# Performance work log

Measured on AMD Instinct MI355X. Metric: run time of the kernel, lower is better.

## Reference

```python
import jax, jax.numpy as jnp
import numpy as np

WIDTH, HEIGHT = 256, 256
FOV = 1.0471975511965976  # 60 deg horizontal fov, radians
Z_NEAR, Z_FAR = 2.0, 6.0
NUM_SAMPLES = 64
HIDDEN = 64


def get_cam_ray_dirs(width, height, horizontal_fov):
    rot_y = jnp.linspace(-horizontal_fov / 2.0, horizontal_fov / 2.0, width)
    vfov = horizontal_fov * height / width
    rot_x = jnp.linspace(vfov / 2.0, -vfov / 2.0, height)
    rot_y = jnp.broadcast_to(rot_y[None, :], (height, width))
    rot_x = jnp.broadcast_to(rot_x[:, None], (height, width))
    x = -jnp.sin(rot_y) * jnp.cos(rot_x)
    y = jnp.sin(rot_x)
    z = -jnp.cos(rot_y) * jnp.cos(rot_x)
    return jnp.stack([x, y, z], axis=2)  # (H, W, 3)


def setup_inputs() -> dict:
    key = jax.random.key(0)
    k1, k2, k3, k4, k5 = jax.random.split(key, 5)
    camera_local_to_world = jax.random.normal(k1, (4, 4), dtype=jnp.float32)
    u = jax.random.uniform(k2, (HEIGHT * WIDTH, NUM_SAMPLES), dtype=jnp.float32)
    cam_ray_dirs = get_cam_ray_dirs(WIDTH, HEIGHT, FOV).astype(jnp.float32)
    W1 = jax.random.normal(k3, (6, HIDDEN), dtype=jnp.float32) * 0.4
    b1 = jnp.zeros((HIDDEN,), dtype=jnp.float32)
    W2 = jax.random.normal(k4, (HIDDEN, 4), dtype=jnp.float32) * 0.1
    b2 = jnp.zeros((4,), dtype=jnp.float32)
    return {"camera_local_to_world": camera_local_to_world, "u": u,
            "cam_ray_dirs": cam_ray_dirs, "W1": W1, "b1": b1, "W2": W2, "b2": b2}


def reference(camera_local_to_world, u, cam_ray_dirs, W1, b1, W2, b2):
    H, W, _ = cam_ray_dirs.shape
    R = H * W
    S = u.shape[1]

    # world-space rays
    rot = camera_local_to_world[:3, :3]
    ray_origin = camera_local_to_world[:3, 3]                    # (3,)
    ray_dirs = jnp.einsum('ij,hwj->hwi', rot, cam_ray_dirs).reshape(R, 3)

    # binned-uniform sample distances along each ray
    dt = Z_FAR - Z_NEAR
    bin_dt = dt / S
    t = jnp.linspace(Z_NEAR, Z_FAR - bin_dt, S, dtype=jnp.float32)[None, :] + u * bin_dt  # (R, S)

    # sample positions and view directions
    pos = ray_origin[None, None, :] + ray_dirs[:, None, :] * t[:, :, None]   # (R, S, 3)
    dirs = jnp.broadcast_to(ray_dirs[:, None, :], (R, S, 3))
    x = jnp.concatenate([pos.reshape(R * S, 3), dirs.reshape(R * S, 3)], axis=1)  # (R*S, 6)

    # radiance MLP: density (non-negative) + rgb color
    h = jax.nn.relu(x @ W1 + b1)                 # (R*S, HIDDEN)
    out = h @ W2 + b2                            # (R*S, 4)
    densities = jax.nn.relu(out[:, 0]).reshape(R, S)
    colors = jax.nn.sigmoid(out[:, 1:]).reshape(R, S, 3)

    # alpha compositing (vectorized form of the back-to-front recurrence:
    # weight_i = alpha_i * prod_{j<i}(1 - alpha_j))
    seps = t[:, 1:] - t[:, :-1]                                   # (R, S-1)
    alphas = 1.0 - jnp.exp(-densities[:, :-1] * seps)             # (R, S-1)
    last_alpha = 1.0 - jnp.exp(-densities[:, -1:] * bin_dt)       # mean_sample_separation = bin_dt
    a = jnp.concatenate([alphas, last_alpha], axis=1)             # (R, S)
    trans = jnp.cumprod(1.0 - a, axis=1)
    T = jnp.concatenate([jnp.ones((R, 1), a.dtype), trans[:, :-1]], axis=1)  # exclusive cumprod
    weights = a * T                                               # (R, S)
    color = jnp.sum(weights[:, :, None] * colors, axis=1)         # (R, 3)
    return color.reshape(H, W, 3)
```

## Files before the change

### kernel.cpp

```cpp
#include <hip/hip_runtime.h>

#define NUM_SAMPLES 64
#define HIDDEN 64
#define Z_NEAR 2.0f
#define Z_FAR 6.0f

typedef _Float16 half8 __attribute__((ext_vector_type(8)));
typedef __fp16  fp16x2 __attribute__((ext_vector_type(2)));
typedef float   float4t __attribute__((ext_vector_type(4)));

template<int CTRL, int RMASK>
__device__ __forceinline__ float dpp_add(float x) {
    const int m = __builtin_amdgcn_update_dpp(0, __float_as_int(x), CTRL, RMASK, 0xf, true);
    return x + __int_as_float(m);
}
__device__ __forceinline__ float wave_scan_add(float x) {
    x = dpp_add<0x111, 0xf>(x);
    x = dpp_add<0x112, 0xf>(x);
    x = dpp_add<0x114, 0xf>(x);
    x = dpp_add<0x118, 0xf>(x);
    x = dpp_add<0x142, 0xa>(x);
    x = dpp_add<0x143, 0xc>(x);
    return x;
}

__global__ __launch_bounds__(256) void render_kernel(
    const float* __restrict__ cam,
    const float* __restrict__ u,
    const float* __restrict__ cdirs,
    const float* __restrict__ W1,
    const float* __restrict__ b1,
    const float* __restrict__ W2,
    const float* __restrict__ b2,
    float* __restrict__ out)
{
    const int lane = threadIdx.x & 63;
    const int wid  = threadIdx.x >> 6;
    const int ray  = blockIdx.x * 4 + wid;
    const int grp  = lane >> 4;
    const int col  = lane & 15;

    __shared__ __align__(16) __fp16 Ahsh[4][HIDDEN];
    __shared__ __align__(16) __fp16 Bhsh[4][HIDDEN];
    __shared__ __align__(16) float  tsh[4][NUM_SAMPLES];
    __shared__ __align__(16) __fp16 W2T[4][4][80];
    __shared__ float cst[4][NUM_SAMPLES * 5];

    {
        const float4 w2row = ((const float4*)W2)[lane];
        W2T[wid][0][lane] = (__fp16)w2row.x;
        W2T[wid][1][lane] = (__fp16)w2row.y;
        W2T[wid][2][lane] = (__fp16)w2row.z;
        W2T[wid][3][lane] = (__fp16)w2row.w;
    }

    const float cd0 = cdirs[ray*3+0], cd1 = cdirs[ray*3+1], cd2 = cdirs[ray*3+2];
    const float rd0 = fmaf(cam[0], cd0, fmaf(cam[1], cd1, cam[2]*cd2));
    const float rd1 = fmaf(cam[4], cd0, fmaf(cam[5], cd1, cam[6]*cd2));
    const float rd2 = fmaf(cam[8], cd0, fmaf(cam[9], cd1, cam[10]*cd2));
    const float o0 = cam[3], o1 = cam[7], o2 = cam[11];

    {
        const int h = lane;
        const float w10 = W1[0*HIDDEN+h], w11 = W1[1*HIDDEN+h], w12 = W1[2*HIDDEN+h];
        const float w13 = W1[3*HIDDEN+h], w14 = W1[4*HIDDEN+h], w15 = W1[5*HIDDEN+h];
        const float A = fmaf(rd0, w10, fmaf(rd1, w11, rd2*w12));
        float B = fmaf(o0, w10, fmaf(o1, w11, o2*w12));
        B = fmaf(rd0, w13, fmaf(rd1, w14, fmaf(rd2, w15, B))) + b1[h];
        Ahsh[wid][lane] = (__fp16)A;
        Bhsh[wid][lane] = (__fp16)B;
    }

    const float bin_dt = (Z_FAR - Z_NEAR) / (float)NUM_SAMPLES;
    const float uv = u[ray*NUM_SAMPLES + lane];
    const float t  = fmaf((float)lane + uv, bin_dt, Z_NEAR);
    tsh[wid][lane] = t;

    union { fp16x2 h2[4]; half8 h8; } aAh[2], aBh[2];
    #pragma unroll
    for (int kt = 0; kt < 2; ++kt) {
        const int h0 = kt*32 + grp*8;
        aAh[kt].h8 = *(const half8*)(&Ahsh[wid][h0]);
        aBh[kt].h8 = *(const half8*)(&Bhsh[wid][h0]);
    }

    half8 bfrag[2] = {};
    if (col < 4) {
        bfrag[0] = *(const half8*)(&W2T[wid][col][grp*8]);
        bfrag[1] = *(const half8*)(&W2T[wid][col][32 + grp*8]);
    }
    const float b2v = b2[col & 3];

    const float tn  = tsh[wid][(lane+1) & 63];
    const float sep = (lane < NUM_SAMPLES-1) ? (tn - t) : bin_dt;

    const fp16x2 hzero = {(__fp16)0.0f, (__fp16)0.0f};

    #pragma unroll
    for (int m = 0; m < 4; ++m) {
        const float tm = tsh[wid][col + 16*m];
        const fp16x2 tvh = __builtin_amdgcn_cvt_pkrtz(tm, tm);
        float4t c = {b2v, b2v, b2v, b2v};
        #pragma unroll
        for (int kt = 0; kt < 2; ++kt) {
            union { fp16x2 h2[4]; half8 h8; } au;
            #pragma unroll
            for (int q = 0; q < 4; ++q) {
                const fp16x2 pre = __builtin_elementwise_fma(aAh[kt].h2[q], tvh, aBh[kt].h2[q]);
                au.h2[q] = __builtin_elementwise_max(pre, hzero);
            }
            c = __builtin_amdgcn_mfma_f32_16x16x32_f16(au.h8, bfrag[kt], c, 0, 0, 0);
        }
        if (col < 4) {
            #pragma unroll
            for (int r = 0; r < 4; ++r) {
                const int sample = 16*m + grp*4 + r;
                cst[wid][sample*5 + col] = c[r];
            }
        }
    }

    const float acc0 = cst[wid][lane*5 + 0];
    const float acc1 = cst[wid][lane*5 + 1];
    const float acc2 = cst[wid][lane*5 + 2];
    const float acc3 = cst[wid][lane*5 + 3];

    const float density = fmaxf(acc0, 0.0f);
    const float dsep  = density * sep;
    const float alpha = 1.0f - __expf(-dsep);
    const float lg    = -dsep * 1.44269504088896f;
    const float S     = wave_scan_add(lg);
    const float T     = exp2f(S - lg);
    const float w     = alpha * T;

    float c0 = w * __builtin_amdgcn_rcpf(1.0f + __expf(-acc1));
    float c1 = w * __builtin_amdgcn_rcpf(1.0f + __expf(-acc2));
    float c2 = w * __builtin_amdgcn_rcpf(1.0f + __expf(-acc3));
    c0 = wave_scan_add(c0);
    c1 = wave_scan_add(c1);
    c2 = wave_scan_add(c2);
    if (lane == 63) {
        out[ray*3+0] = c0;
        out[ray*3+1] = c1;
        out[ray*3+2] = c2;
    }
}

extern "C" void kernel_launch(void* const* d_in, const int* in_sizes, int n_in,
                              void* d_out, int out_size, void* d_ws, size_t ws_size,
                              hipStream_t stream) {
    const float* cam   = (const float*)d_in[0];
    const float* u     = (const float*)d_in[1];
    const float* cdirs = (const float*)d_in[2];
    const float* W1    = (const float*)d_in[3];
    const float* b1    = (const float*)d_in[4];
    const float* W2    = (const float*)d_in[5];
    const float* b2    = (const float*)d_in[6];
    float* out = (float*)d_out;

    const int R = 256 * 256;
    dim3 grid(R / 4), block(256);
    render_kernel<<<grid, block, 0, stream>>>(cam, u, cdirs, W1, b1, W2, b2, out);
}
```

Measured before the change: 30.30 us.

## Process eight rays per wave with prefetch and hoisted per-wave setup

Each wave now loops over eight rays instead of handling one, so the W1/b1/W2 loads, the W2 transpose into shared memory and the camera reads happen once per wave rather than once per ray. The next ray's u and direction values are prefetched during the current iteration to hide load latency. Camera parameters are broadcast via readlane, and the exponentials use native exp2 with explicit log2e scaling. This trades grid-level parallelism (fewer blocks) for less redundant setup work, and adds an occupancy hint to launch bounds.

```diff
diff --git a/kernel.cpp b/kernel.cpp
--- a/kernel.cpp
+++ b/kernel.cpp
@@ -4,6 +4,7 @@
 #define HIDDEN 64
 #define Z_NEAR 2.0f
 #define Z_FAR 6.0f
+#define RPW 8
 
 typedef _Float16 half8 __attribute__((ext_vector_type(8)));
 typedef __fp16  fp16x2 __attribute__((ext_vector_type(2)));
@@ -24,7 +25,9 @@
     return x;
 }
 
-__global__ __launch_bounds__(256) void render_kernel(
+#define LOG2E 1.44269504088896f
+
+__global__ __launch_bounds__(256, 8) void render_kernel(
     const float* __restrict__ cam,
     const float* __restrict__ u,
     const float* __restrict__ cdirs,
@@ -36,7 +39,7 @@
 {
     const int lane = threadIdx.x & 63;
     const int wid  = threadIdx.x >> 6;
-    const int ray  = blockIdx.x * 4 + wid;
+    const int wave = blockIdx.x * 4 + wid;
     const int grp  = lane >> 4;
     const int col  = lane & 15;
 
@@ -54,95 +57,116 @@
         W2T[wid][3][lane] = (__fp16)w2row.w;
     }
 
-    const float cd0 = cdirs[ray*3+0], cd1 = cdirs[ray*3+1], cd2 = cdirs[ray*3+2];
-    const float rd0 = fmaf(cam[0], cd0, fmaf(cam[1], cd1, cam[2]*cd2));
-    const float rd1 = fmaf(cam[4], cd0, fmaf(cam[5], cd1, cam[6]*cd2));
-    const float rd2 = fmaf(cam[8], cd0, fmaf(cam[9], cd1, cam[10]*cd2));
-    const float o0 = cam[3], o1 = cam[7], o2 = cam[11];
+    const float cl = (lane < 12) ? cam[lane] : 0.0f;
+    float camv[12];
+    #pragma unroll
+    for (int i = 0; i < 12; ++i)
+        camv[i] = __int_as_float(__builtin_amdgcn_readlane(__float_as_int(cl), i));
 
-    {
-        const int h = lane;
-        const float w10 = W1[0*HIDDEN+h], w11 = W1[1*HIDDEN+h], w12 = W1[2*HIDDEN+h];
-        const float w13 = W1[3*HIDDEN+h], w14 = W1[4*HIDDEN+h], w15 = W1[5*HIDDEN+h];
-        const float A = fmaf(rd0, w10, fmaf(rd1, w11, rd2*w12));
-        float B = fmaf(o0, w10, fmaf(o1, w11, o2*w12));
-        B = fmaf(rd0, w13, fmaf(rd1, w14, fmaf(rd2, w15, B))) + b1[h];
-        Ahsh[wid][lane] = (__fp16)A;
-        Bhsh[wid][lane] = (__fp16)B;
-    }
-
-    const float bin_dt = (Z_FAR - Z_NEAR) / (float)NUM_SAMPLES;
-    const float uv = u[ray*NUM_SAMPLES + lane];
-    const float t  = fmaf((float)lane + uv, bin_dt, Z_NEAR);
-    tsh[wid][lane] = t;
-
-    union { fp16x2 h2[4]; half8 h8; } aAh[2], aBh[2];
-    #pragma unroll
-    for (int kt = 0; kt < 2; ++kt) {
-        const int h0 = kt*32 + grp*8;
-        aAh[kt].h8 = *(const half8*)(&Ahsh[wid][h0]);
-        aBh[kt].h8 = *(const half8*)(&Bhsh[wid][h0]);
-    }
+    const float w10 = W1[0*HIDDEN+lane], w11 = W1[1*HIDDEN+lane], w12 = W1[2*HIDDEN+lane];
+    const float w13 = W1[3*HIDDEN+lane], w14 = W1[4*HIDDEN+lane], w15 = W1[5*HIDDEN+lane];
+    const float b1h = b1[lane];
+    const float b2v = b2[col & 3];
 
     half8 bfrag[2] = {};
     if (col < 4) {
         bfrag[0] = *(const half8*)(&W2T[wid][col][grp*8]);
         bfrag[1] = *(const half8*)(&W2T[wid][col][32 + grp*8]);
     }
-    const float b2v = b2[col & 3];
 
-    const float tn  = tsh[wid][(lane+1) & 63];
-    const float sep = (lane < NUM_SAMPLES-1) ? (tn - t) : bin_dt;
-
+    const float bin_dt = (Z_FAR - Z_NEAR) / (float)NUM_SAMPLES;
     const fp16x2 hzero = {(__fp16)0.0f, (__fp16)0.0f};
 
-    #pragma unroll
-    for (int m = 0; m < 4; ++m) {
-        const float tm = tsh[wid][col + 16*m];
-        const fp16x2 tvh = __builtin_amdgcn_cvt_pkrtz(tm, tm);
-        float4t c = {b2v, b2v, b2v, b2v};
+    int ray = wave * RPW;
+    float uv  = u[ray*NUM_SAMPLES + lane];
+    float cd0 = cdirs[ray*3+0], cd1 = cdirs[ray*3+1], cd2 = cdirs[ray*3+2];
+
+    for (int it = 0; it < RPW; ++it, ++ray) {
+        float uv_n = 0.f, cd0_n = 0.f, cd1_n = 0.f, cd2_n = 0.f;
+        if (it < RPW-1) {
+            uv_n  = u[(ray+1)*NUM_SAMPLES + lane];
+            cd0_n = cdirs[(ray+1)*3+0];
+            cd1_n = cdirs[(ray+1)*3+1];
+            cd2_n = cdirs[(ray+1)*3+2];
+        }
+
+        const float rd0 = fmaf(camv[0], cd0, fmaf(camv[1], cd1, camv[2]*cd2));
+        const float rd1 = fmaf(camv[4], cd0, fmaf(camv[5], cd1, camv[6]*cd2));
+        const float rd2 = fmaf(camv[8], cd0, fmaf(camv[9], cd1, camv[10]*cd2));
+        const float o0 = camv[3], o1 = camv[7], o2 = camv[11];
+
+        {
+            const float A = fmaf(rd0, w10, fmaf(rd1, w11, rd2*w12));
+            float B = fmaf(o0, w10, fmaf(o1, w11, o2*w12));
+            B = fmaf(rd0, w13, fmaf(rd1, w14, fmaf(rd2, w15, B))) + b1h;
+            Ahsh[wid][lane] = (__fp16)A;
+            Bhsh[wid][lane] = (__fp16)B;
+        }
+
+        const float t = fmaf((float)lane + uv, bin_dt, Z_NEAR);
+        tsh[wid][lane] = t;
+
+        union { fp16x2 h2[4]; half8 h8; } aAh[2], aBh[2];
         #pragma unroll
         for (int kt = 0; kt < 2; ++kt) {
-            union { fp16x2 h2[4]; half8 h8; } au;
+            const int h0 = kt*32 + grp*8;
+            aAh[kt].h8 = *(const half8*)(&Ahsh[wid][h0]);
+            aBh[kt].h8 = *(const half8*)(&Bhsh[wid][h0]);
+        }
+
+        const float tn  = tsh[wid][(lane+1) & 63];
+        const float sep = (lane < NUM_SAMPLES-1) ? (tn - t) : bin_dt;
+
+        #pragma unroll
+        for (int m = 0; m < 4; ++m) {
+            const float tm = tsh[wid][col + 16*m];
+            const fp16x2 tvh = __builtin_amdgcn_cvt_pkrtz(tm, tm);
+            float4t c = {b2v, b2v, b2v, b2v};
             #pragma unroll
-            for (int q = 0; q < 4; ++q) {
-                const fp16x2 pre = __builtin_elementwise_fma(aAh[kt].h2[q], tvh, aBh[kt].h2[q]);
-                au.h2[q] = __builtin_elementwise_max(pre, hzero);
+            for (int kt = 0; kt < 2; ++kt) {
+                union { fp16x2 h2[4]; half8 h8; } au;
+                #pragma unroll
+                for (int q = 0; q < 4; ++q) {
+                    const fp16x2 pre = __builtin_elementwise_fma(aAh[kt].h2[q], tvh, aBh[kt].h2[q]);
+                    au.h2[q] = __builtin_elementwise_max(pre, hzero);
+                }
+                c = __builtin_amdgcn_mfma_f32_16x16x32_f16(au.h8, bfrag[kt], c, 0, 0, 0);
             }
-            c = __builtin_amdgcn_mfma_f32_16x16x32_f16(au.h8, bfrag[kt], c, 0, 0, 0);
-        }
-        if (col < 4) {
-            #pragma unroll
-            for (int r = 0; r < 4; ++r) {
-                const int sample = 16*m + grp*4 + r;
-                cst[wid][sample*5 + col] = c[r];
+            if (col < 4) {
+                #pragma unroll
+                for (int r = 0; r < 4; ++r) {
+                    const int sample = 16*m + grp*4 + r;
+                    cst[wid][sample*5 + col] = c[r];
+                }
             }
         }
-    }
 
-    const float acc0 = cst[wid][lane*5 + 0];
-    const float acc1 = cst[wid][lane*5 + 1];
-    const float acc2 = cst[wid][lane*5 + 2];
-    const float acc3 = cst[wid][lane*5 + 3];
+        const float acc0 = cst[wid][lane*5 + 0];
+        const float acc1 = cst[wid][lane*5 + 1];
+        const float acc2 = cst[wid][lane*5 + 2];
+        const float acc3 = cst[wid][lane*5 + 3];
 
-    const float density = fmaxf(acc0, 0.0f);
-    const float dsep  = density * sep;
-    const float alpha = 1.0f - __expf(-dsep);
-    const float lg    = -dsep * 1.44269504088896f;
-    const float S     = wave_scan_add(lg);
-    const float T     = exp2f(S - lg);
-    const float w     = alpha * T;
+        const float density = fmaxf(acc0, 0.0f);
+        const float dsep  = density * sep;
+        const float lg    = -dsep * LOG2E;
+        const float alpha = 1.0f - __builtin_amdgcn_exp2f(lg);
+        const float S     = wave_scan_add(lg);
+        const float T     = __builtin_amdgcn_exp2f(S - lg);
+        const float w     = alpha * T;
 
-    float c0 = w * __builtin_amdgcn_rcpf(1.0f + __expf(-acc1));
-    float c1 = w * __builtin_amdgcn_rcpf(1.0f + __expf(-acc2));
-    float c2 = w * __builtin_amdgcn_rcpf(1.0f + __expf(-acc3));
-    c0 = wave_scan_add(c0);
-    c1 = wave_scan_add(c1);
-    c2 = wave_scan_add(c2);
-    if (lane == 63) {
-        out[ray*3+0] = c0;
-        out[ray*3+1] = c1;
-        out[ray*3+2] = c2;
+        float c0 = w * __builtin_amdgcn_rcpf(1.0f + __builtin_amdgcn_exp2f(-acc1 * LOG2E));
+        float c1 = w * __builtin_amdgcn_rcpf(1.0f + __builtin_amdgcn_exp2f(-acc2 * LOG2E));
+        float c2 = w * __builtin_amdgcn_rcpf(1.0f + __builtin_amdgcn_exp2f(-acc3 * LOG2E));
+        c0 = wave_scan_add(c0);
+        c1 = wave_scan_add(c1);
+        c2 = wave_scan_add(c2);
+        if (lane == 63) {
+            out[ray*3+0] = c0;
+            out[ray*3+1] = c1;
+            out[ray*3+2] = c2;
+        }
+
+        uv = uv_n; cd0 = cd0_n; cd1 = cd1_n; cd2 = cd2_n;
     }
 }
 
@@ -158,7 +182,6 @@
     const float* b2    = (const float*)d_in[6];
     float* out = (float*)d_out;
 
-    const int R = 256 * 256;
-    dim3 grid(R / 4), block(256);
+    dim3 grid(2048), block(256);
     render_kernel<<<grid, block, 0, stream>>>(cam, u, cdirs, W1, b1, W2, b2, out);
 }
```

After: 33.37 us. 10.1% more time.
